# Optimization experiments

Hardware: AMD Instinct MI355X
Metric: run time of the kernel (lower is better)

The kernel has to match this reference:

```python
import jax, jax.numpy as jnp
import numpy as np

K, D, SIGMA, SC, EPS = 13, 3, 9.0, 0.1, 1e-5
DEPTH, DIM, HEADS = 6, 256, 8
B, H, W = 1, 48, 64


def _win_start(L, k, d):
    # NATTEN dilated neighborhood window start (static, numpy).
    nb = k // 2
    idx = np.arange(L)
    if d <= 1:
        return np.maximum(idx - nb, 0) + (idx + nb >= L) * (L - idx - nb - 1)
    imodd = idx % d
    a = (L // d) * d
    b = L - a
    right = np.where(imodd < b, L - b + imodd - 2 * nb * d, a + imodd - k * d)
    return np.where(idx - nb * d < 0, imodd,
                    np.where(idx + nb * d >= L, right, idx - nb * d))


def _pb_start(L, k, d):
    # NATTEN relative-position-bias start index (static, numpy).
    nb = k // 2
    idx = np.arange(L)
    if d <= 1:
        return nb + (idx < nb) * (nb - idx) + (idx + nb >= L) * (L - idx - 1 - nb)
    return np.where(idx - nb * d < 0, k - 1 - idx // d,
                    np.where(idx + nb * d >= L, (L - idx - 1) // d, nb))


def _layernorm(x, w, b):
    m = x.mean(-1, keepdims=True)
    v = ((x - m) ** 2).mean(-1, keepdims=True)
    return (x - m) * jax.lax.rsqrt(v + EPS) * w + b


def _ga(x, qkv_w, qkv_b, rpb_l, lr_m_l, proj_w_l, proj_b_l):
    # x: (B,H,W,C) -> neighborhood attention with RPB + learned gaussian mask.
    b, h, w, c = x.shape
    hd = c // HEADS
    scale = hd ** -0.5
    qkv = (x @ qkv_w.T + qkv_b).reshape(b, h, w, 3, HEADS, hd)
    qkv = jnp.transpose(qkv, (3, 0, 4, 1, 2, 5))  # (3,B,n,H,W,d)
    q, k, v = qkv[0] * scale, qkv[1], qkv[2]
    sh, sw = _win_start(h, K, D), _win_start(w, K, D)
    ph, pw = _pb_start(h, K, D), _pb_start(w, K, D)
    taps = np.arange(K)
    ih = sh[:, None] + D * taps  # (H,K) key rows per query row
    iw = sw[:, None] + D * taps  # (W,K)
    kg = k[:, :, ih][:, :, :, :, iw]  # (B,n,H,K,W,K,d)
    vg = v[:, :, ih][:, :, :, :, iw]
    attn = jnp.einsum('bnhwd,bnhiwjd->bnhwij', q, kg)  # (B,n,H,W,K,K)
    bi = ph[:, None] + taps
    bj = pw[:, None] + taps
    bias = rpb_l[:, bi][:, :, :, bj]  # (n,H,K,W,K)
    attn = attn + jnp.transpose(bias, (0, 1, 3, 2, 4))[None]
    crd = jnp.arange(K, dtype=x.dtype)
    g = jnp.exp(-((crd[None, :] - K // 2) ** 2 + (crd[:, None] - K // 2) ** 2)
                / (2.0 * SIGMA ** 2))
    ker = g + lr_m_l / SC  # (K,K)
    attn = attn * ker[None, None, None, None]
    attn = jax.nn.softmax(attn.reshape(b, HEADS, h, w, K * K), axis=-1)
    attn = attn.reshape(b, HEADS, h, w, K, K)
    out = jnp.einsum('bnhwij,bnhiwjd->bnhwd', attn, vg)
    out = jnp.transpose(out, (0, 2, 3, 1, 4)).reshape(b, h, w, c)
    return out @ proj_w_l.T + proj_b_l


def setup_inputs() -> dict:
    key = jax.random.key(0)
    ks = jax.random.split(key, 8)
    s = 0.02
    return {
        'x': jax.random.normal(ks[0], (B, DIM, H, W), jnp.float32),
        'ln1_w': jnp.ones((DEPTH, DIM), jnp.float32),
        'ln1_b': jnp.zeros((DEPTH, DIM), jnp.float32),
        'qkv_w': jax.random.normal(ks[1], (DEPTH, 3 * DIM, DIM), jnp.float32) * s,
        'qkv_b': jnp.zeros((DEPTH, 3 * DIM), jnp.float32),
        'rpb': jax.random.normal(ks[2], (DEPTH, HEADS, 2 * K - 1, 2 * K - 1), jnp.float32) * s,
        'lr_m': jnp.ones((DEPTH, K, K), jnp.float32) * (SC * 0.5),
        'proj_w': jax.random.normal(ks[3], (DEPTH, DIM, DIM), jnp.float32) * s,
        'proj_b': jnp.zeros((DEPTH, DIM), jnp.float32),
        'ln2_w': jnp.ones((DEPTH, DIM), jnp.float32),
        'ln2_b': jnp.zeros((DEPTH, DIM), jnp.float32),
        'fc1_w': jax.random.normal(ks[4], (DEPTH, 4 * DIM, DIM), jnp.float32) * s,
        'fc1_b': jnp.zeros((DEPTH, 4 * DIM), jnp.float32),
        'fc2_w': jax.random.normal(ks[5], (DEPTH, DIM, 4 * DIM), jnp.float32) * s,
        'fc2_b': jnp.zeros((DEPTH, DIM), jnp.float32),
        'normf_w': jnp.ones((DIM,), jnp.float32),
        'normf_b': jnp.zeros((DIM,), jnp.float32),
    }


def reference(x, ln1_w, ln1_b, qkv_w, qkv_b, rpb, lr_m, proj_w, proj_b,
              ln2_w, ln2_b, fc1_w, fc1_b, fc2_w, fc2_b, normf_w, normf_b):
    b, c, h, w = x.shape
    t = jnp.transpose(x, (0, 2, 3, 1)).reshape(b, h * w, c)
    for l in range(ln1_w.shape[0]):
        shortcut = t
        y = _layernorm(t, ln1_w[l], ln1_b[l]).reshape(b, h, w, c)
        y = _ga(y, qkv_w[l], qkv_b[l], rpb[l], lr_m[l], proj_w[l], proj_b[l])
        t = shortcut + y.reshape(b, h * w, c)
        m = _layernorm(t, ln2_w[l], ln2_b[l])
        m = jax.nn.gelu(m @ fc1_w[l].T + fc1_b[l], approximate=False)
        m = m @ fc2_w[l].T + fc2_b[l]
        t = t + m
    t = _layernorm(t, normf_w, normf_b)
    return jnp.transpose(t.reshape(b, h, w, c), (0, 3, 1, 2))
```

## Files before the change

### kernel.cpp

```cpp
#include <hip/hip_runtime.h>
#include <hip/hip_bf16.h>
#include <math.h>

#define DIMC   256
#define HH     48
#define WW     64
#define MROWS  (HH*WW)
#define NHEADS 8
#define HD     32
#define KTAP   13
#define NTAPS  (KTAP*KTAP)
#define DIL    3
#define NB     6
#define EPSLN  1e-5f
#define QSCALE 0.17677669529663687f

typedef __attribute__((ext_vector_type(8))) short bf16x8;
typedef __attribute__((ext_vector_type(4))) float f32x4;
typedef _Float16 __f16;
typedef __f16 f16x2 __attribute__((ext_vector_type(2)));

__device__ __forceinline__ f16x2 pkh(float a, float b) {
    auto r = __builtin_amdgcn_cvt_pkrtz(a, b);
    return __builtin_bit_cast(f16x2, r);
}
__device__ __forceinline__ f16x2 bch(unsigned u) {
    return __builtin_bit_cast(f16x2, u);
}

__device__ __forceinline__ int win_start(int i, int L) {
    int imodd = i % DIL;
    if (i - NB * DIL < 0) return imodd;
    if (i + NB * DIL >= L) {
        int a = (L / DIL) * DIL;
        int b = L - a;
        if (imodd < b) return L - b + imodd - 2 * NB * DIL;
        return a + imodd - KTAP * DIL;
    }
    return i - NB * DIL;
}
__device__ __forceinline__ int pb_start(int i, int L) {
    if (i - NB * DIL < 0) return KTAP - 1 - i / DIL;
    if (i + NB * DIL >= L) return (L - 1 - i) / DIL;
    return NB;
}

__global__ __launch_bounds__(256) void cvt_all_kernel(const float* __restrict__ w0,
                                                      const float* __restrict__ w1,
                                                      const float* __restrict__ w2,
                                                      const float* __restrict__ w3,
                                                      __hip_bfloat16* __restrict__ o0,
                                                      __hip_bfloat16* __restrict__ o1,
                                                      __hip_bfloat16* __restrict__ o2,
                                                      __hip_bfloat16* __restrict__ o3) {
    int i = blockIdx.x * 256 + threadIdx.x;
    const float* in;
    __hip_bfloat16* out;
    int off;
    if (i < 294912)      { in = w0; out = o0; off = i; }
    else if (i < 393216) { in = w1; out = o1; off = i - 294912; }
    else if (i < 786432) { in = w2; out = o2; off = i - 393216; }
    else                 { in = w3; out = o3; off = i - 786432; }
    float4 v = ((const float4*)in)[off];
    union { __hip_bfloat16 h[4]; ushort4 u; } p;
    p.h[0] = __float2bfloat16(v.x);
    p.h[1] = __float2bfloat16(v.y);
    p.h[2] = __float2bfloat16(v.z);
    p.h[3] = __float2bfloat16(v.w);
    ((ushort4*)out)[off] = p.u;
}

__global__ void transpose_in_kernel(const float* __restrict__ x, float* __restrict__ t) {
    int m = blockIdx.x;
    int c = threadIdx.x;
    t[m * DIMC + c] = x[c * MROWS + m];
}

template <typename OutT, int TRANS>
__global__ __launch_bounds__(256) void ln_kernel(const float* __restrict__ in,
                                                 const float* __restrict__ w,
                                                 const float* __restrict__ b,
                                                 OutT* __restrict__ out) {
    __shared__ float s1[4], s2[4];
    int m = blockIdx.x;
    int c = threadIdx.x;
    float v = in[m * DIMC + c];
    float a = v, q = v * v;
    #pragma unroll
    for (int o = 32; o > 0; o >>= 1) {
        a += __shfl_xor(a, o);
        q += __shfl_xor(q, o);
    }
    if ((threadIdx.x & 63) == 0) { s1[threadIdx.x >> 6] = a; s2[threadIdx.x >> 6] = q; }
    __syncthreads();
    float mean = (s1[0] + s1[1] + s1[2] + s1[3]) * (1.0f / DIMC);
    float var  = (s2[0] + s2[1] + s2[2] + s2[3]) * (1.0f / DIMC) - mean * mean;
    float r = (v - mean) * rsqrtf(var + EPSLN) * w[c] + b[c];
    if (TRANS) {
        out[c * MROWS + m] = (OutT)r;
    } else {
        if constexpr (sizeof(OutT) == 2) out[m * DIMC + c] = __float2bfloat16(r);
        else                             out[m * DIMC + c] = r;
    }
}

#define LDP 72
template <int EPI, typename OutT>
__global__ __launch_bounds__(256) void gemm_mfma_kernel(const __hip_bfloat16* __restrict__ A,
                                                        const __hip_bfloat16* __restrict__ Wt,
                                                        const float* __restrict__ bias,
                                                        const float* __restrict__ res,
                                                        OutT* __restrict__ C,
                                                        int M, int N, int K) {
    __shared__ __hip_bfloat16 As[64][LDP];
    __shared__ __hip_bfloat16 Ws[64][LDP];
    int tid = threadIdx.x;
    int bm = blockIdx.y * 64, bn = blockIdx.x * 64;
    int lane = tid & 63, wid = tid >> 6;
    int wr = wid >> 1, wc = wid & 1;
    int fr = lane & 15, fq = lane >> 4;
    f32x4 acc[2][2] = {};

    uint2 ra[4], rw[4];
    #pragma unroll
    for (int i = 0; i < 4; i++) {
        int idx = tid + i * 256;
        int r = idx >> 4, c = (idx & 15) << 2;
        ra[i] = *(const uint2*)&A[(size_t)(bm + r) * K + c];
        rw[i] = *(const uint2*)&Wt[(size_t)(bn + r) * K + c];
    }

    for (int k0 = 0; k0 < K; k0 += 64) {
        #pragma unroll
        for (int i = 0; i < 4; i++) {
            int idx = tid + i * 256;
            int r = idx >> 4, c = (idx & 15) << 2;
            *(uint2*)&As[r][c] = ra[i];
            *(uint2*)&Ws[r][c] = rw[i];
        }
        __syncthreads();
        if (k0 + 64 < K) {
            #pragma unroll
            for (int i = 0; i < 4; i++) {
                int idx = tid + i * 256;
                int r = idx >> 4, c = (idx & 15) << 2;
                ra[i] = *(const uint2*)&A[(size_t)(bm + r) * K + k0 + 64 + c];
                rw[i] = *(const uint2*)&Wt[(size_t)(bn + r) * K + k0 + 64 + c];
            }
        }
        #pragma unroll
        for (int kk = 0; kk < 2; kk++) {
            int kb = kk * 32 + fq * 8;
            bf16x8 af[2], bfr[2];
            #pragma unroll
            for (int i = 0; i < 2; i++) {
                union { uint4 u; bf16x8 v; } ua, ub;
                ua.u = *(const uint4*)&As[wr * 32 + i * 16 + fr][kb];
                af[i] = ua.v;
                ub.u = *(const uint4*)&Ws[wc * 32 + i * 16 + fr][kb];
                bfr[i] = ub.v;
            }
            #pragma unroll
            for (int i = 0; i < 2; i++)
                #pragma unroll
                for (int j = 0; j < 2; j++)
                    acc[i][j] = __builtin_amdgcn_mfma_f32_16x16x32_bf16(
                        af[i], bfr[j], acc[i][j], 0, 0, 0);
        }
        __syncthreads();
    }
    #pragma unroll
    for (int i = 0; i < 2; i++) {
        int mbase = bm + wr * 32 + i * 16 + fq * 4;
        #pragma unroll
        for (int j = 0; j < 2; j++) {
            int n = bn + wc * 32 + j * 16 + fr;
            float bv = bias[n];
            #pragma unroll
            for (int r = 0; r < 4; r++) {
                int m = mbase + r;
                float v = acc[i][j][r] + bv;
                if (EPI == 1) v = v * 0.5f * (1.0f + erff(v * 0.70710678118654752f));
                if (EPI == 2) v += res[(size_t)m * N + n];
                if constexpr (sizeof(OutT) == 2) C[(size_t)m * N + n] = __float2bfloat16(v);
                else                             C[(size_t)m * N + n] = v;
            }
        }
    }
}

__global__ __launch_bounds__(512, 4) void attn_kernel(const float* __restrict__ qkv,
                                                      const float* __restrict__ rpb,
                                                      const float* __restrict__ lrm,
                                                      __hip_bfloat16* __restrict__ out) {
    __shared__ __align__(16) unsigned KVd[KTAP * WW * 20];
    __shared__ float rpbs[625];
    __shared__ float kers[NTAPS];

    int tid = threadIdx.x;
    int h = blockIdx.x >> 3;
    int n = blockIdx.x & 7;
    int q = tid >> 3;
    int c = tid & 7;
    int shh = win_start(h, HH);
    int ph  = pb_start(h, HH);
    int sww = win_start(q, WW);
    int pwq = pb_start(q, WW);
    int mrow = h * WW + q;

    for (int i = tid; i < 625; i += 512) rpbs[i] = rpb[n * 625 + i];
    if (tid < NTAPS) {
        int ti = tid / KTAP, tj = tid - KTAP * ti;
        float dx = (float)(tj - NB), dy = (float)(ti - NB);
        kers[tid] = __expf(-(dx * dx + dy * dy) * (1.0f / 162.0f)) + lrm[tid] * 10.0f;
    }

    float4 kreg[14], qv[8];
    #pragma unroll
    for (int it = 0; it < 7; ++it) {
        int tau = tid + 512 * it;
        if (tau < 3328) {
            int row = tau >> 2, j = tau & 3;
            int ti0 = row >> 6, col = row & 63;
            int ihr = shh + DIL * ti0;
            const float4* g = (const float4*)(qkv + (size_t)(ihr * WW + col) * 768
                                              + DIMC + n * HD + 8 * j);
            kreg[2 * it] = g[0]; kreg[2 * it + 1] = g[1];
        }
    }
    {
        const float4* qg = (const float4*)(qkv + (size_t)mrow * 768 + n * HD);
        #pragma unroll
        for (int i = 0; i < 8; ++i) qv[i] = qg[i];
    }

    #pragma unroll
    for (int it = 0; it < 7; ++it) {
        int tau = tid + 512 * it;
        if (tau < 3328) {
            int row = tau >> 2, j = tau & 3;
            float4 u0 = kreg[2 * it], u1 = kreg[2 * it + 1];
            uint4 w;
            w.x = __builtin_bit_cast(unsigned, pkh(u0.x, u0.y));
            w.y = __builtin_bit_cast(unsigned, pkh(u0.z, u0.w));
            w.z = __builtin_bit_cast(unsigned, pkh(u1.x, u1.y));
            w.w = __builtin_bit_cast(unsigned, pkh(u1.z, u1.w));
            *(uint4*)&KVd[row * 20 + j * 4] = w;
        }
    }
    f16x2 qh[16];
    #pragma unroll
    for (int i = 0; i < 8; ++i) {
        qh[2 * i]     = pkh(qv[i].x * QSCALE, qv[i].y * QSCALE);
        qh[2 * i + 1] = pkh(qv[i].z * QSCALE, qv[i].w * QSCALE);
    }
    __syncthreads();

    float4 vA[6];
    #pragma unroll
    for (int it = 0; it < 3; ++it) {
        int tau = tid + 512 * it;
        int row = tau >> 2, j = tau & 3;
        int ti0 = row >> 6, col = row & 63;
        int ihr = shh + DIL * ti0;
        const float4* g = (const float4*)(qkv + (size_t)(ihr * WW + col) * 768
                                          + 2 * DIMC + n * HD + 8 * j);
        vA[2 * it] = g[0]; vA[2 * it + 1] = g[1];
    }

    float p[22];
    float smax = -1e30f;
    {
        int ti = 0, tj = c, tt = c;
        int row = sww + 3 * c;
        #pragma unroll
        for (int k = 0; k < 22; ++k) {
            if (tt < NTAPS) {
                const unsigned* kp = KVd + row * 20;
                uint4 r0 = *(const uint4*)(kp);
                uint4 r1 = *(const uint4*)(kp + 4);
                uint4 r2 = *(const uint4*)(kp + 8);
                uint4 r3 = *(const uint4*)(kp + 12);
                f16x2 sa = {}, sb = {}, sc2 = {}, sd = {};
                sa  += qh[0]  * bch(r0.x); sb  += qh[1]  * bch(r0.y);
                sc2 += qh[2]  * bch(r0.z); sd  += qh[3]  * bch(r0.w);
                sa  += qh[4]  * bch(r1.x); sb  += qh[5]  * bch(r1.y);
                sc2 += qh[6]  * bch(r1.z); sd  += qh[7]  * bch(r1.w);
                sa  += qh[8]  * bch(r2.x); sb  += qh[9]  * bch(r2.y);
                sc2 += qh[10] * bch(r2.z); sd  += qh[11] * bch(r2.w);
                sa  += qh[12] * bch(r3.x); sb  += qh[13] * bch(r3.y);
                sc2 += qh[14] * bch(r3.z); sd  += qh[15] * bch(r3.w);
                f16x2 st = (sa + sb) + (sc2 + sd);
                float s = (float)st.x + (float)st.y;
                s += rpbs[(ph + ti) * 25 + pwq + tj];
                s *= kers[tt];
                p[k] = s;
                smax = fmaxf(smax, s);
            } else {
                p[k] = -1e30f;
            }
            tj += 8; row += 24;
            if (tj >= KTAP) { tj -= KTAP; ++ti; row += 25; }
            tt += 8;
        }
    }
    __syncthreads();

    #pragma unroll
    for (int it = 0; it < 3; ++it) {
        int tau = tid + 512 * it;
        int row = tau >> 2, j = tau & 3;
        float4 u0 = vA[2 * it], u1 = vA[2 * it + 1];
        uint4 w;
        w.x = __builtin_bit_cast(unsigned, pkh(u0.x, u0.y));
        w.y = __builtin_bit_cast(unsigned, pkh(u0.z, u0.w));
        w.z = __builtin_bit_cast(unsigned, pkh(u1.x, u1.y));
        w.w = __builtin_bit_cast(unsigned, pkh(u1.z, u1.w));
        *(uint4*)&KVd[row * 20 + j * 4] = w;
    }
    float4 vB[8];
    #pragma unroll
    for (int it = 3; it < 7; ++it) {
        int tau = tid + 512 * it;
        if (tau < 3328) {
            int row = tau >> 2, j = tau & 3;
            int ti0 = row >> 6, col = row & 63;
            int ihr = shh + DIL * ti0;
            const float4* g = (const float4*)(qkv + (size_t)(ihr * WW + col) * 768
                                              + 2 * DIMC + n * HD + 8 * j);
            vB[2 * (it - 3)] = g[0]; vB[2 * (it - 3) + 1] = g[1];
        }
    }

    #pragma unroll
    for (int o = 1; o < 8; o <<= 1) smax = fmaxf(smax, __shfl_xor(smax, o));
    float ssum = 0.0f;
    #pragma unroll
    for (int k = 0; k < 22; ++k) {
        float e = __expf(p[k] - smax);
        p[k] = e;
        ssum += e;
    }
    #pragma unroll
    for (int o = 1; o < 8; o <<= 1) ssum += __shfl_xor(ssum, o);
    float inv = 1.0f / ssum;
    #pragma unroll
    for (int k = 0; k < 22; ++k) p[k] *= inv;

    #pragma unroll
    for (int it = 3; it < 7; ++it) {
        int tau = tid + 512 * it;
        if (tau < 3328) {
            int row = tau >> 2, j = tau & 3;
            float4 u0 = vB[2 * (it - 3)], u1 = vB[2 * (it - 3) + 1];
            uint4 w;
            w.x = __builtin_bit_cast(unsigned, pkh(u0.x, u0.y));
            w.y = __builtin_bit_cast(unsigned, pkh(u0.z, u0.w));
            w.z = __builtin_bit_cast(unsigned, pkh(u1.x, u1.y));
            w.w = __builtin_bit_cast(unsigned, pkh(u1.z, u1.w));
            *(uint4*)&KVd[row * 20 + j * 4] = w;
        }
    }
    __syncthreads();

    f16x2 acc2[16] = {};
    {
        int ti = 0, tj = c, tt = c;
        int row = sww + 3 * c;
        #pragma unroll
        for (int k = 0; k < 22; ++k) {
            if (tt < NTAPS) {
                const unsigned* vp = KVd + row * 20;
                uint4 r0 = *(const uint4*)(vp);
                uint4 r1 = *(const uint4*)(vp + 4);
                uint4 r2 = *(const uint4*)(vp + 8);
                uint4 r3 = *(const uint4*)(vp + 12);
                f16x2 p2 = pkh(p[k], p[k]);
                acc2[0]  += p2 * bch(r0.x); acc2[1]  += p2 * bch(r0.y);
                acc2[2]  += p2 * bch(r0.z); acc2[3]  += p2 * bch(r0.w);
                acc2[4]  += p2 * bch(r1.x); acc2[5]  += p2 * bch(r1.y);
                acc2[6]  += p2 * bch(r1.z); acc2[7]  += p2 * bch(r1.w);
                acc2[8]  += p2 * bch(r2.x); acc2[9]  += p2 * bch(r2.y);
                acc2[10] += p2 * bch(r2.z); acc2[11] += p2 * bch(r2.w);
                acc2[12] += p2 * bch(r3.x); acc2[13] += p2 * bch(r3.y);
                acc2[14] += p2 * bch(r3.z); acc2[15] += p2 * bch(r3.w);
            }
            tj += 8; row += 24;
            if (tj >= KTAP) { tj -= KTAP; ++ti; row += 25; }
            tt += 8;
        }
    }
    f16x2 r8v[8];
    {
        bool b = (c & 4);
        #pragma unroll
        for (int i = 0; i < 8; ++i) {
            f16x2 keep = b ? acc2[i + 8] : acc2[i];
            f16x2 send = b ? acc2[i] : acc2[i + 8];
            float sf = __shfl_xor(__builtin_bit_cast(float, send), 4);
            r8v[i] = keep + __builtin_bit_cast(f16x2, sf);
        }
    }
    f16x2 r4v[4];
    {
        bool b = (c & 2);
        #pragma unroll
        for (int i = 0; i < 4; ++i) {
            f16x2 keep = b ? r8v[i + 4] : r8v[i];
            f16x2 send = b ? r8v[i] : r8v[i + 4];
            float sf = __shfl_xor(__builtin_bit_cast(float, send), 2);
            r4v[i] = keep + __builtin_bit_cast(f16x2, sf);
        }
    }
    f16x2 r2v[2];
    {
        bool b = (c & 1);
        #pragma unroll
        for (int i = 0; i < 2; ++i) {
            f16x2 keep = b ? r4v[i + 2] : r4v[i];
            f16x2 send = b ? r4v[i] : r4v[i + 2];
            float sf = __shfl_xor(__builtin_bit_cast(float, send), 1);
            r2v[i] = keep + __builtin_bit_cast(f16x2, sf);
        }
    }
    union { __hip_bfloat16 hh[4]; ushort4 u4; } ow;
    ow.hh[0] = __float2bfloat16((float)r2v[0].x);
    ow.hh[1] = __float2bfloat16((float)r2v[0].y);
    ow.hh[2] = __float2bfloat16((float)r2v[1].x);
    ow.hh[3] = __float2bfloat16((float)r2v[1].y);
    *(ushort4*)&out[(size_t)mrow * DIMC + n * HD + c * 4] = ow.u4;
}

extern "C" void kernel_launch(void* const* d_in, const int* in_sizes, int n_in,
                              void* d_out, int out_size, void* d_ws, size_t ws_size,
                              hipStream_t stream) {
    const float* x      = (const float*)d_in[0];
    const float* ln1_w  = (const float*)d_in[1];
    const float* ln1_b  = (const float*)d_in[2];
    const float* qkv_w  = (const float*)d_in[3];
    const float* qkv_b  = (const float*)d_in[4];
    const float* rpb    = (const float*)d_in[5];
    const float* lr_m   = (const float*)d_in[6];
    const float* proj_w = (const float*)d_in[7];
    const float* proj_b = (const float*)d_in[8];
    const float* ln2_w  = (const float*)d_in[9];
    const float* ln2_b  = (const float*)d_in[10];
    const float* fc1_w  = (const float*)d_in[11];
    const float* fc1_b  = (const float*)d_in[12];
    const float* fc2_w  = (const float*)d_in[13];
    const float* fc2_b  = (const float*)d_in[14];
    const float* nf_w   = (const float*)d_in[15];
    const float* nf_b   = (const float*)d_in[16];
    float* out = (float*)d_out;

    char* ws = (char*)d_ws;
    float*          t        = (float*)ws;
    float*          qkvb     = (float*)(ws + 3145728);
    __hip_bfloat16* y        = (__hip_bfloat16*)(ws + 12582912);
    __hip_bfloat16* attn_out = (__hip_bfloat16*)(ws + 14155776);
    __hip_bfloat16* m1       = (__hip_bfloat16*)(ws + 15728640);
    __hip_bfloat16* qkv_wb   = (__hip_bfloat16*)(ws + 22020096);
    __hip_bfloat16* proj_wb  = (__hip_bfloat16*)(ws + 24379392);
    __hip_bfloat16* fc1_wb   = (__hip_bfloat16*)(ws + 25165824);
    __hip_bfloat16* fc2_wb   = (__hip_bfloat16*)(ws + 28311552);

    cvt_all_kernel<<<1179648 / 256, 256, 0, stream>>>(
        qkv_w, proj_w, fc1_w, fc2_w, qkv_wb, proj_wb, fc1_wb, fc2_wb);

    transpose_in_kernel<<<MROWS, 256, 0, stream>>>(x, t);

    for (int l = 0; l < 6; l++) {
        const __hip_bfloat16* qw  = qkv_wb  + (size_t)l * 768 * 256;
        const __hip_bfloat16* pw  = proj_wb + (size_t)l * 256 * 256;
        const __hip_bfloat16* f1w = fc1_wb  + (size_t)l * 1024 * 256;
        const __hip_bfloat16* f2w = fc2_wb  + (size_t)l * 256 * 1024;
        const float* qb  = qkv_b  + (size_t)l * 768;
        const float* pb  = proj_b + (size_t)l * 256;
        const float* f1b = fc1_b  + (size_t)l * 1024;
        const float* f2b = fc2_b  + (size_t)l * 256;
        const float* rp  = rpb    + (size_t)l * NHEADS * 25 * 25;
        const float* lm  = lr_m   + (size_t)l * NTAPS;

        ln_kernel<__hip_bfloat16, 0><<<MROWS, 256, 0, stream>>>(
            t, ln1_w + l * 256, ln1_b + l * 256, y);
        gemm_mfma_kernel<0, float><<<dim3(768 / 64, MROWS / 64), 256, 0, stream>>>(
            y, qw, qb, nullptr, qkvb, MROWS, 768, 256);
        attn_kernel<<<HH * NHEADS, 512, 0, stream>>>(qkvb, rp, lm, attn_out);
        gemm_mfma_kernel<2, float><<<dim3(256 / 64, MROWS / 64), 256, 0, stream>>>(
            attn_out, pw, pb, t, t, MROWS, 256, 256);
        ln_kernel<__hip_bfloat16, 0><<<MROWS, 256, 0, stream>>>(
            t, ln2_w + l * 256, ln2_b + l * 256, y);
        gemm_mfma_kernel<1, __hip_bfloat16><<<dim3(1024 / 64, MROWS / 64), 256, 0, stream>>>(
            y, f1w, f1b, nullptr, m1, MROWS, 1024, 256);
        gemm_mfma_kernel<2, float><<<dim3(256 / 64, MROWS / 64), 256, 0, stream>>>(
            m1, f2w, f2b, t, t, MROWS, 256, 1024);
    }

    ln_kernel<float, 1><<<MROWS, 256, 0, stream>>>(t, nf_w, nf_b, out);
}
```

Before: 399.0 us.

## Fuse LayerNorm into the A-operand load of the QKV and FC1 GEMMs

Removes the two standalone LayerNorm kernels per layer. The QKV and FC1 GEMMs now read fp32 rows of t directly, compute mean and variance per row across 4 threads, normalize, round to bf16 and stage the result into shared memory. This drops two launches per layer and the write and read of the bf16 y buffer. In exchange, every column-block recomputes LayerNorm for its 64 rows, so A is read 12 or 16 times as fp32, and register pressure rises from holding a full 256-wide row segment per thread.

```diff
diff --git a/kernel.cpp b/kernel.cpp
--- a/kernel.cpp
+++ b/kernel.cpp
@@ -26,6 +26,10 @@
 }
 __device__ __forceinline__ f16x2 bch(unsigned u) {
     return __builtin_bit_cast(f16x2, u);
+}
+__device__ __forceinline__ unsigned short bf16rn(float x) {
+    union { float f; unsigned u; } cv; cv.f = x;
+    return (unsigned short)((cv.u + 0x7fff + ((cv.u >> 16) & 1)) >> 16);
 }
 
 __device__ __forceinline__ int win_start(int i, int L) {
@@ -76,11 +80,10 @@
     t[m * DIMC + c] = x[c * MROWS + m];
 }
 
-template <typename OutT, int TRANS>
-__global__ __launch_bounds__(256) void ln_kernel(const float* __restrict__ in,
-                                                 const float* __restrict__ w,
-                                                 const float* __restrict__ b,
-                                                 OutT* __restrict__ out) {
+__global__ __launch_bounds__(256) void ln_final_kernel(const float* __restrict__ in,
+                                                       const float* __restrict__ w,
+                                                       const float* __restrict__ b,
+                                                       float* __restrict__ out) {
     __shared__ float s1[4], s2[4];
     int m = blockIdx.x;
     int c = threadIdx.x;
@@ -96,12 +99,7 @@
     float mean = (s1[0] + s1[1] + s1[2] + s1[3]) * (1.0f / DIMC);
     float var  = (s2[0] + s2[1] + s2[2] + s2[3]) * (1.0f / DIMC) - mean * mean;
     float r = (v - mean) * rsqrtf(var + EPSLN) * w[c] + b[c];
-    if (TRANS) {
-        out[c * MROWS + m] = (OutT)r;
-    } else {
-        if constexpr (sizeof(OutT) == 2) out[m * DIMC + c] = __float2bfloat16(r);
-        else                             out[m * DIMC + c] = r;
-    }
+    out[c * MROWS + m] = r;
 }
 
 #define LDP 72
@@ -182,6 +180,126 @@
                 float v = acc[i][j][r] + bv;
                 if (EPI == 1) v = v * 0.5f * (1.0f + erff(v * 0.70710678118654752f));
                 if (EPI == 2) v += res[(size_t)m * N + n];
+                if constexpr (sizeof(OutT) == 2) C[(size_t)m * N + n] = __float2bfloat16(v);
+                else                             C[(size_t)m * N + n] = v;
+            }
+        }
+    }
+}
+
+template <int EPI, typename OutT>
+__global__ __launch_bounds__(256) void gemm_lnA_kernel(const float* __restrict__ A,
+                                                       const float* __restrict__ lnw,
+                                                       const float* __restrict__ lnb,
+                                                       const __hip_bfloat16* __restrict__ Wt,
+                                                       const float* __restrict__ bias,
+                                                       OutT* __restrict__ C,
+                                                       int M, int N) {
+    __shared__ __hip_bfloat16 As[64][LDP];
+    __shared__ __hip_bfloat16 Ws[64][LDP];
+    int tid = threadIdx.x;
+    int bm = blockIdx.y * 64, bn = blockIdx.x * 64;
+    int ar = tid >> 2;
+    int g  = tid & 3;
+
+    uint2 an[16];
+    {
+        float4 av[16];
+        const float4* ag = (const float4*)(A + (size_t)(bm + ar) * 256);
+        float s = 0.0f, ss = 0.0f;
+        #pragma unroll
+        for (int i = 0; i < 16; i++) {
+            float4 v = ag[g + 4 * i];
+            av[i] = v;
+            s  += v.x + v.y + v.z + v.w;
+            ss += v.x * v.x + v.y * v.y + v.z * v.z + v.w * v.w;
+        }
+        s  += __shfl_xor(s, 1);  s  += __shfl_xor(s, 2);
+        ss += __shfl_xor(ss, 1); ss += __shfl_xor(ss, 2);
+        float mean = s * (1.0f / 256.0f);
+        float var  = ss * (1.0f / 256.0f) - mean * mean;
+        float rstd = rsqrtf(var + EPSLN);
+        const float4* wg = (const float4*)lnw;
+        const float4* bg = (const float4*)lnb;
+        #pragma unroll
+        for (int i = 0; i < 16; i++) {
+            float4 w4 = wg[g + 4 * i], b4 = bg[g + 4 * i];
+            unsigned short h0 = bf16rn((av[i].x - mean) * rstd * w4.x + b4.x);
+            unsigned short h1 = bf16rn((av[i].y - mean) * rstd * w4.y + b4.y);
+            unsigned short h2 = bf16rn((av[i].z - mean) * rstd * w4.z + b4.z);
+            unsigned short h3 = bf16rn((av[i].w - mean) * rstd * w4.w + b4.w);
+            an[i].x = (unsigned)h0 | ((unsigned)h1 << 16);
+            an[i].y = (unsigned)h2 | ((unsigned)h3 << 16);
+        }
+    }
+
+    int lane = tid & 63, wid = tid >> 6;
+    int wr = wid >> 1, wc = wid & 1;
+    int fr = lane & 15, fq = lane >> 4;
+    f32x4 acc[2][2] = {};
+
+    uint2 rw[4];
+    #pragma unroll
+    for (int i = 0; i < 4; i++) {
+        int idx = tid + i * 256;
+        int r = idx >> 4, c = (idx & 15) << 2;
+        rw[i] = *(const uint2*)&Wt[(size_t)(bn + r) * 256 + c];
+    }
+
+    #pragma unroll
+    for (int t = 0; t < 4; t++) {
+        #pragma unroll
+        for (int j = 0; j < 4; j++) {
+            *(uint2*)&As[ar][4 * g + 16 * j] = an[4 * t + j];
+        }
+        #pragma unroll
+        for (int i = 0; i < 4; i++) {
+            int idx = tid + i * 256;
+            int r = idx >> 4, c = (idx & 15) << 2;
+            *(uint2*)&Ws[r][c] = rw[i];
+        }
+        __syncthreads();
+        if (t < 3) {
+            #pragma unroll
+            for (int i = 0; i < 4; i++) {
+                int idx = tid + i * 256;
+                int r = idx >> 4, c = (idx & 15) << 2;
+                rw[i] = *(const uint2*)&Wt[(size_t)(bn + r) * 256 + (t + 1) * 64 + c];
+            }
+        }
+        #pragma unroll
+        for (int kk = 0; kk < 2; kk++) {
+            int kb = kk * 32 + fq * 8;
+            bf16x8 af[2], bfr[2];
+            #pragma unroll
+            for (int i = 0; i < 2; i++) {
+                union { uint4 u; bf16x8 v; } ua, ub;
+                ua.u = *(const uint4*)&As[wr * 32 + i * 16 + fr][kb];
+                af[i] = ua.v;
+                ub.u = *(const uint4*)&Ws[wc * 32 + i * 16 + fr][kb];
+                bfr[i] = ub.v;
+            }
+            #pragma unroll
+            for (int i = 0; i < 2; i++)
+                #pragma unroll
+                for (int j = 0; j < 2; j++)
+                    acc[i][j] = __builtin_amdgcn_mfma_f32_16x16x32_bf16(
+                        af[i], bfr[j], acc[i][j], 0, 0, 0);
+        }
+        __syncthreads();
+    }
+    #pragma unroll
+    for (int i = 0; i < 2; i++) {
+        int mbase = bm + wr * 32 + i * 16 + fq * 4;
+        #pragma unroll
+        for (int j = 0; j < 2; j++) {
+            int n = bn + wc * 32 + j * 16 + fr;
+            float bv = bias[n];
+            #pragma unroll
+            for (int r = 0; r < 4; r++) {
+                int m = mbase + r;
+                float v = acc[i][j][r] + bv;
+                if (EPI == 1) v = v * 0.5f * (1.0f + erff(v * 0.70710678118654752f));
                 if constexpr (sizeof(OutT) == 2) C[(size_t)m * N + n] = __float2bfloat16(v);
                 else                             C[(size_t)m * N + n] = v;
             }
@@ -456,7 +574,6 @@
     char* ws = (char*)d_ws;
     float*          t        = (float*)ws;
     float*          qkvb     = (float*)(ws + 3145728);
-    __hip_bfloat16* y        = (__hip_bfloat16*)(ws + 12582912);
     __hip_bfloat16* attn_out = (__hip_bfloat16*)(ws + 14155776);
     __hip_bfloat16* m1       = (__hip_bfloat16*)(ws + 15728640);
     __hip_bfloat16* qkv_wb   = (__hip_bfloat16*)(ws + 22020096);
@@ -481,20 +598,16 @@
         const float* rp  = rpb    + (size_t)l * NHEADS * 25 * 25;
         const float* lm  = lr_m   + (size_t)l * NTAPS;
 
-        ln_kernel<__hip_bfloat16, 0><<<MROWS, 256, 0, stream>>>(
-            t, ln1_w + l * 256, ln1_b + l * 256, y);
-        gemm_mfma_kernel<0, float><<<dim3(768 / 64, MROWS / 64), 256, 0, stream>>>(
-            y, qw, qb, nullptr, qkvb, MROWS, 768, 256);
+        gemm_lnA_kernel<0, float><<<dim3(768 / 64, MROWS / 64), 256, 0, stream>>>(
+            t, ln1_w + l * 256, ln1_b + l * 256, qw, qb, qkvb, MROWS, 768);
         attn_kernel<<<HH * NHEADS, 512, 0, stream>>>(qkvb, rp, lm, attn_out);
         gemm_mfma_kernel<2, float><<<dim3(256 / 64, MROWS / 64), 256, 0, stream>>>(
             attn_out, pw, pb, t, t, MROWS, 256, 256);
-        ln_kernel<__hip_bfloat16, 0><<<MROWS, 256, 0, stream>>>(
-            t, ln2_w + l * 256, ln2_b + l * 256, y);
-        gemm_mfma_kernel<1, __hip_bfloat16><<<dim3(1024 / 64, MROWS / 64), 256, 0, stream>>>(
-            y, f1w, f1b, nullptr, m1, MROWS, 1024, 256);
+        gemm_lnA_kernel<1, __hip_bfloat16><<<dim3(1024 / 64, MROWS / 64), 256, 0, stream>>>(
+            t, ln2_w + l * 256, ln2_b + l * 256, f1w, f1b, m1, MROWS, 1024);
         gemm_mfma_kernel<2, float><<<dim3(256 / 64, MROWS / 64), 256, 0, stream>>>(
             m1, f2w, f2b, t, t, MROWS, 256, 1024);
     }
 
-    ln_kernel<float, 1><<<MROWS, 256, 0, stream>>>(t, nf_w, nf_b, out);
-}
+    ln_final_kernel<<<MROWS, 256, 0, stream>>>(t, nf_w, nf_b, out);
+}
```

Measured after the change: 423.8 us. 1.06x slower.
